# Performance work log

Measured on AMD Instinct MI355X. Metric: run time of the kernel, lower is better.

## Reference

```python
import jax, jax.numpy as jnp
import numpy as np

N_ITEMS = 50000
N_USERS = 20000
N_NODES = N_ITEMS + N_USERS
D = 128
N_REL = 3
NNZ = 800000
K_LAYERS = 2
B, S, L = 256, 4, 50


def setup_inputs() -> dict:
    key = jax.random.key(0)
    ks = iter(jax.random.split(key, 40))
    stdv = float(1.0 / np.sqrt(D))

    def uni(shape):
        return jax.random.uniform(next(ks), shape, jnp.float32, -stdv, stdv)

    id_emb = (jax.random.normal(next(ks), (N_ITEMS, D), jnp.float32) * 0.1).at[0].set(0.0)  # padding_idx=0
    user_emb = jax.random.normal(next(ks), (N_USERS, D), jnp.float32) * 0.1
    inp = dict(
        id_emb=id_emb, user_emb=user_emb,
        lin_r_w=uni((K_LAYERS, N_REL, D, D)),
        upi_w=uni((K_LAYERS, D, D)), upi_b=uni((K_LAYERS, D)),
        upu_w=uni((K_LAYERS, D, D)), upu_b=uni((K_LAYERS, D)),
        w_ih=uni((3 * D, 2 * D)), w_hh=uni((3 * D, D)),
        b_ih=uni((3 * D,)), b_hh=uni((3 * D,)),
        b_iah=uni((D,)), b_oah=uni((D,)),
        ei_w=uni((D, D)), ei_b=uni((D,)),
        eo_w=uni((D, D)), eo_b=uni((D,)),
        q1_w=uni((D, D)), q2_w=uni((D, D)), att_w=uni((D,)),
        fuse_w=uni((D, 2 * D)), fuse_b=uni((D,)),
    )
    # global heterogeneous graph: COO per relation over item+user nodes
    inp['rel_rows'] = jax.random.randint(next(ks), (N_REL, NNZ), 0, N_NODES, dtype=jnp.int32)
    inp['rel_cols'] = jax.random.randint(next(ks), (N_REL, NNZ), 0, N_NODES, dtype=jnp.int32)
    inp['rel_vals'] = jax.random.uniform(next(ks), (N_REL, NNZ), jnp.float32) * 0.1
    # session batch: every session has length in [2, L]
    lens = jax.random.randint(next(ks), (B, S), 2, L + 1)
    raw = jax.random.randint(next(ks), (B, S, L), 1, N_ITEMS)
    inp['ids'] = (raw * (jnp.arange(L)[None, None, :] < lens[:, :, None])).astype(jnp.int32)
    inp['uid'] = jax.random.randint(next(ks), (B,), 0, N_USERS, dtype=jnp.int32)
    inp['u_type'] = jax.random.randint(next(ks), (B,), 0, 3).astype(jnp.float32)
    return inp


def _hgnn(h_item, h_user, rel_rows, rel_cols, rel_vals, lin_r_w, upi_w, upi_b, upu_w, upu_b):
    Ni = h_item.shape[0]
    N = Ni + h_user.shape[0]
    for k in range(lin_r_w.shape[0]):
        h_all = jnp.concatenate([h_item, h_user], 0)
        msg = jnp.zeros_like(h_all)
        for r in range(rel_rows.shape[0]):
            Wh = h_all @ lin_r_w[k, r].T  # per-relation linear
            msg = msg + jax.ops.segment_sum(Wh[rel_cols[r]] * rel_vals[r][:, None],
                                            rel_rows[r], num_segments=N)  # sparse.mm
        h_item = jax.nn.relu((msg[:Ni] + h_item) @ upi_w[k].T + upi_b[k])
        h_user = jax.nn.relu((msg[Ni:] + h_user) @ upu_w[k].T + upu_b[k])
    return h_item, h_user


def reference(id_emb, user_emb, lin_r_w, upi_w, upi_b, upu_w, upu_b,
              w_ih, w_hh, b_ih, b_hh, b_iah, b_oah,
              ei_w, ei_b, eo_w, eo_b, q1_w, q2_w, att_w, fuse_w, fuse_b,
              rel_rows, rel_cols, rel_vals, ids, uid, u_type):
    Bb, Ss, Ll = ids.shape
    N = Ss * Bb
    ids_sb = jnp.transpose(ids, (1, 0, 2)).reshape(N, Ll)  # session-major, matches torch concat order
    lens = (ids_sb != 0).sum(-1)  # >= 2 by construction -> all sessions valid
    rows = jnp.arange(N)
    target = ids_sb[rows, lens - 1]
    Lp = Ll - 1
    m_in = jnp.arange(Lp)[None, :] < (lens - 1)[:, None]
    seq_in = ids_sb[:, :Lp] * m_in
    # session graph: consecutive-item edges; in-half sub-diagonal, out-half super-diagonal
    valid = (m_in[:, 1:] & m_in[:, :-1]).astype(jnp.float32)  # [N, Lp-1]
    i1 = jnp.arange(1, Lp)
    i0 = jnp.arange(Lp - 1)
    a_in = jnp.zeros((N, Lp, Lp), jnp.float32).at[:, i1, i0].set(valid)
    a_out = jnp.zeros((N, Lp, Lp), jnp.float32).at[:, i0, i1].set(valid)
    deg = jnp.clip(a_in.sum(-1), 1.0, None)[..., None]
    a_in = a_in / deg
    a_out = a_out / deg
    h = id_emb[seq_in]  # [N, Lp, D]
    # SessionGNN GRU-style cell (step=1)
    m_i = jnp.matmul(a_in, h @ ei_w.T + ei_b) + b_iah
    m_o = jnp.matmul(a_out, h @ eo_w.T + eo_b) + b_oah
    gi = jnp.concatenate([m_i, m_o], -1) @ w_ih.T + b_ih
    gh = h @ w_hh.T + b_hh
    i_r, i_i, i_n = jnp.split(gi, 3, -1)
    h_r, h_i, h_n = jnp.split(gh, 3, -1)
    rg = jax.nn.sigmoid(i_r + h_r)
    zg = jax.nn.sigmoid(i_i + h_i)
    ng = jnp.tanh(i_n + rg * h_n)
    h = ng + zg * (h - ng)
    # attention readout
    ht = h[rows, jnp.clip(lens - 2, 0, None)]
    alpha = jax.nn.sigmoid((ht @ q1_w.T)[:, None, :] + h @ q2_w.T) @ att_w  # [N, Lp]
    alpha = alpha * m_in.astype(jnp.float32)
    alpha = alpha / (alpha.sum(1, keepdims=True) + 1e-8)
    c_cur = jnp.einsum('nl,nld->nd', alpha, h)
    # global HGNN user context
    g_item, g_user = _hgnn(id_emb[:N_ITEMS], user_emb[:N_USERS], rel_rows, rel_cols,
                           rel_vals, lin_r_w, upi_w, upi_b, upu_w, upu_b)
    c_hist = g_user[jnp.tile(uid, Ss)]
    reps = jnp.concatenate([c_cur, c_hist], -1) @ fuse_w.T + fuse_b
    return reps, target, jnp.tile(u_type, Ss)
```

## Files before the change

kernel.cpp:

```cpp
#include <hip/hip_runtime.h>
#include <hip/hip_bf16.h>

typedef __hip_bfloat16 bf16;
typedef unsigned int uint32;
typedef __attribute__((ext_vector_type(8))) short short8;
typedef __attribute__((ext_vector_type(4))) float f32x4;
typedef __attribute__((ext_vector_type(2))) float f32x2;
typedef __attribute__((ext_vector_type(4))) uint32 u32x4;

#define N_ITEMS_C 50000
#define N_USERS_C 20000
#define N_NODES_C 70000
#define NNZ_C 800000
#define NSESS 1024
#define LP 49
#define NTOK (NSESS * LP)
#define NBK 137

__device__ __forceinline__ float bflo(uint32 u) { return __uint_as_float(u << 16); }
__device__ __forceinline__ float bfhi(uint32 u) { return __uint_as_float(u & 0xffff0000u); }
__device__ __forceinline__ float bfhi_fast(uint32 u) { return __uint_as_float(u); }
__device__ __forceinline__ uint32 packbf(float a, float b) {
    return (uint32)__bfloat16_as_ushort(__float2bfloat16(a)) |
           ((uint32)__bfloat16_as_ushort(__float2bfloat16(b)) << 16);
}

__global__ void init_hab_kernel(const float4* __restrict__ idp, const float4* __restrict__ usp,
                                uint32* __restrict__ hab) {
    int i = blockIdx.x * 256 + threadIdx.x;
    float4 w = (i < 1600000) ? idp[i] : usp[i - 1600000];
    uint2 o = make_uint2(packbf(w.x, w.y), packbf(w.z, w.w));
    *(uint2*)&hab[(size_t)i * 2] = o;
}

__global__ __launch_bounds__(256) void bucket_hist_kernel(
    const int* __restrict__ rel_rows, int* __restrict__ bhist)
{
    __shared__ int hist[NBK];
    const int r = blockIdx.y, tid = threadIdx.x;
    if (tid < NBK) hist[tid] = 0;
    __syncthreads();
    const int* rr = rel_rows + (size_t)r * NNZ_C;
#pragma unroll
    for (int i = 0; i < 16; ++i) {
        int e = blockIdx.x * 4096 + i * 256 + tid;
        if (e < NNZ_C) atomicAdd(&hist[rr[e] >> 9], 1);
    }
    __syncthreads();
    if (tid < NBK && hist[tid]) atomicAdd(&bhist[r * NBK + tid], hist[tid]);
}

__global__ __launch_bounds__(256) void bucket_scan_kernel(
    const int* __restrict__ bhist, int* __restrict__ bbase)
{
    __shared__ int s[256];
    const int tid = threadIdx.x;
    for (int r = 0; r < 3; ++r) {
        s[tid] = (tid < NBK) ? bhist[r * NBK + tid] : 0;
        __syncthreads();
        for (int d = 1; d < 256; d <<= 1) {
            int t = (tid >= d) ? s[tid - d] : 0;
            __syncthreads();
            s[tid] += t;
            __syncthreads();
        }
        if (tid < NBK) bbase[r * (NBK + 1) + tid + 1] = s[tid];
        if (tid == 0) bbase[r * (NBK + 1)] = 0;
        __syncthreads();
    }
}

__global__ __launch_bounds__(256) void bucket_scatter_kernel(
    const int* __restrict__ rel_rows, const int* __restrict__ rel_cols,
    const float* __restrict__ rel_vals, const int* __restrict__ bbase,
    int* __restrict__ cursor, int2* __restrict__ tmp)
{
    __shared__ int hist[NBK], gbase[NBK], cur2[NBK];
    const int r = blockIdx.y, tid = threadIdx.x;
    if (tid < NBK) { hist[tid] = 0; cur2[tid] = 0; }
    __syncthreads();
    const int* rr = rel_rows + (size_t)r * NNZ_C;
    const int* rc = rel_cols + (size_t)r * NNZ_C;
    const float* rv = rel_vals + (size_t)r * NNZ_C;
    int rows[16];
#pragma unroll
    for (int i = 0; i < 16; ++i) {
        int e = blockIdx.x * 4096 + i * 256 + tid;
        rows[i] = (e < NNZ_C) ? rr[e] : -1;
        if (rows[i] >= 0) atomicAdd(&hist[rows[i] >> 9], 1);
    }
    __syncthreads();
    if (tid < NBK)
        gbase[tid] = bbase[r * (NBK + 1) + tid] +
                     (hist[tid] ? atomicAdd(&cursor[r * NBK + tid], hist[tid]) : 0);
    __syncthreads();
    int2* tp = tmp + (size_t)r * NNZ_C;
#pragma unroll
    for (int i = 0; i < 16; ++i) {
        int e = blockIdx.x * 4096 + i * 256 + tid;
        if (rows[i] >= 0) {
            int bk = rows[i] >> 9;
            int rank = atomicAdd(&cur2[bk], 1);
            uint32 fb = __float_as_uint(rv[e]);
            uint32 pk = (uint32)rc[e] | (((fb >> 16) & 0x7FFFu) << 17);
            tp[gbase[bk] + rank] = make_int2((int)pk, rows[i]);
        }
    }
}

__global__ __launch_bounds__(256) void bucket_refine_kernel(
    const int2* __restrict__ tmp, const int* __restrict__ bbase,
    int* __restrict__ offs, uint32* __restrict__ edges)
{
    __shared__ int cnt[512], offsL[512], cur[512];
    __shared__ uint32 outb[6656];
    const int b = blockIdx.x, r = blockIdx.y, tid = threadIdx.x;
    const int lane = tid & 63, wid = tid >> 6;
    const int row0 = b << 9;
    const int e0 = bbase[r * (NBK + 1) + b];
    const int e1 = bbase[r * (NBK + 1) + b + 1];
    cnt[tid] = 0; cnt[256 + tid] = 0; cur[tid] = 0; cur[256 + tid] = 0;
    __syncthreads();
    const int2* tp = tmp + (size_t)r * NNZ_C;
    for (int e = e0 + tid; e < e1; e += 256)
        atomicAdd(&cnt[tp[e].y - row0], 1);
    __syncthreads();
    if (wid == 0) {
        int carry = 0;
        for (int c = 0; c < 8; ++c) {
            int x = cnt[c * 64 + lane];
            int inc = x;
#pragma unroll
            for (int d = 1; d < 64; d <<= 1) {
                int y = __shfl_up(inc, d, 64);
                if (lane >= d) inc += y;
            }
            offsL[c * 64 + lane] = inc - x + carry;
            carry += __shfl(inc, 63, 64);
        }
    }
    __syncthreads();
    for (int i = tid; i < 512; i += 256) {
        int row = row0 + i;
        if (row < 70001) offs[(size_t)r * 70001 + row] = e0 + offsL[i];
    }
    for (int e = e0 + tid; e < e1; e += 256) {
        int2 E = tp[e];
        int lr_ = E.y - row0;
        int slot = offsL[lr_] + atomicAdd(&cur[lr_], 1);
        if (slot < 6656) outb[slot] = (uint32)E.x;
    }
    __syncthreads();
    uint32* eo = edges + (size_t)r * NNZ_C + e0;
    for (int i = tid; i < e1 - e0; i += 256) eo[i] = outb[i];
}

__global__ __launch_bounds__(256) void gather_kernel(
    const uint32* __restrict__ hab, const uint32* __restrict__ edges,
    const int* __restrict__ offs, uint32* __restrict__ T)
{
    const int row = blockIdx.x * 4 + (threadIdx.x >> 6);
    const int lane = threadIdx.x & 63;
    const int grp = lane >> 4;
    const int ql  = lane & 15;
    const char* __restrict__ habB = (const char*)hab + ql * 16;
    f32x2 acc[3][4];
#pragma unroll
    for (int r = 0; r < 3; ++r)
#pragma unroll
        for (int j = 0; j < 4; ++j) acc[r][j] = (f32x2){0.f, 0.f};
#pragma unroll
    for (int r = 0; r < 3; ++r) {
        const uint32* __restrict__ ed = edges + (size_t)r * NNZ_C;
        const int* __restrict__ of = offs + (size_t)r * 70001;
        const int e0 = of[row], e1 = of[row + 1];
        if (e0 >= e1) continue;
        const uint32 span = (uint32)(e1 - e0);
        const int s0 = e0 & ~3;
        for (int eb = s0; eb < e1; eb += 16) {
            const int base = eb + grp * 4;
            uint4 E4 = *(const uint4*)&ed[base];
            uint32 Ej0 = ((uint32)(base + 0 - e0) < span) ? E4.x : 0u;
            uint32 Ej1 = ((uint32)(base + 1 - e0) < span) ? E4.y : 0u;
            uint32 Ej2 = ((uint32)(base + 2 - e0) < span) ? E4.z : 0u;
            uint32 Ej3 = ((uint32)(base + 3 - e0) < span) ? E4.w : 0u;
            uint4 u0 = *(const uint4*)(habB + ((Ej0 & 0x1FFFFu) << 8));
            uint4 u1 = *(const uint4*)(habB + ((Ej1 & 0x1FFFFu) << 8));
            uint4 u2 = *(const uint4*)(habB + ((Ej2 & 0x1FFFFu) << 8));
            uint4 u3 = *(const uint4*)(habB + ((Ej3 & 0x1FFFFu) << 8));
            float v0 = __uint_as_float((Ej0 >> 1) & 0x7FFF0000u);
            float v1 = __uint_as_float((Ej1 >> 1) & 0x7FFF0000u);
            float v2 = __uint_as_float((Ej2 >> 1) & 0x7FFF0000u);
            float v3 = __uint_as_float((Ej3 >> 1) & 0x7FFF0000u);
            f32x2 vv;
            vv = (f32x2){v0, v0};
            acc[r][0] += vv * (f32x2){bflo(u0.x), bfhi_fast(u0.x)};
            acc[r][1] += vv * (f32x2){bflo(u0.y), bfhi_fast(u0.y)};
            acc[r][2] += vv * (f32x2){bflo(u0.z), bfhi_fast(u0.z)};
            acc[r][3] += vv * (f32x2){bflo(u0.w), bfhi_fast(u0.w)};
            vv = (f32x2){v1, v1};
            acc[r][0] += vv * (f32x2){bflo(u1.x), bfhi_fast(u1.x)};
            acc[r][1] += vv * (f32x2){bflo(u1.y), bfhi_fast(u1.y)};
            acc[r][2] += vv * (f32x2){bflo(u1.z), bfhi_fast(u1.z)};
            acc[r][3] += vv * (f32x2){bflo(u1.w), bfhi_fast(u1.w)};
            vv = (f32x2){v2, v2};
            acc[r][0] += vv * (f32x2){bflo(u2.x), bfhi_fast(u2.x)};
            acc[r][1] += vv * (f32x2){bflo(u2.y), bfhi_fast(u2.y)};
            acc[r][2] += vv * (f32x2){bflo(u2.z), bfhi_fast(u2.z)};
            acc[r][3] += vv * (f32x2){bflo(u2.w), bfhi_fast(u2.w)};
            vv = (f32x2){v3, v3};
            acc[r][0] += vv * (f32x2){bflo(u3.x), bfhi_fast(u3.x)};
            acc[r][1] += vv * (f32x2){bflo(u3.y), bfhi_fast(u3.y)};
            acc[r][2] += vv * (f32x2){bflo(u3.z), bfhi_fast(u3.z)};
            acc[r][3] += vv * (f32x2){bflo(u3.w), bfhi_fast(u3.w)};
        }
    }
    float* af = (float*)acc;
#pragma unroll
    for (int off = 16; off < 64; off <<= 1)
#pragma unroll
        for (int j = 0; j < 24; ++j) af[j] += __shfl_xor(af[j], off, 64);
    if (grp == 0) {
#pragma unroll
        for (int r = 0; r < 3; ++r) {
            u32x4 o;
            o.x = packbf(acc[r][0].x, acc[r][0].y);
            o.y = packbf(acc[r][1].x, acc[r][1].y);
            o.z = packbf(acc[r][2].x, acc[r][2].y);
            o.w = packbf(acc[r][3].x, acc[r][3].y);
            __builtin_nontemporal_store(o, (u32x4*)&T[(size_t)row * 192 + r * 64 + ql * 4]);
        }
    }
}

__global__ __launch_bounds__(256, 3) void wprep_kernel(
    const float* __restrict__ upi_w, const float* __restrict__ upu_w,
    const float* __restrict__ lin_r_w, int k, uint32* __restrict__ Wcat)
{
    __shared__ float As[128][65];
    __shared__ __align__(8) bf16 Ws[128][66];
    const int which = blockIdx.y, seg = which / 3, r = which % 3;
    const float* U  = (seg == 0 ? upi_w : upu_w) + (size_t)k * 16384;
    const float* Wr = lin_r_w + (size_t)(k * 3 + r) * 16384;
    uint32* out = Wcat + (size_t)seg * 32768;
    const int tid = threadIdx.x;
    const int row0 = blockIdx.x * 64;
#pragma unroll
    for (int i = 0; i < 8; ++i) {
        int id = i * 256 + tid;
        int rr = id >> 5, c4 = (id & 31) << 2;
        float4 v = *(const float4*)&U[(size_t)(row0 + rr) * 128 + c4];
        As[c4][rr] = v.x; As[c4+1][rr] = v.y; As[c4+2][rr] = v.z; As[c4+3][rr] = v.w;
    }
    const int m0 = (tid & 15) * 4;
    const int n0 = (tid >> 4) * 8;
    float acc[4][8];
#pragma unroll
    for (int i = 0; i < 4; ++i)
#pragma unroll
        for (int j = 0; j < 8; ++j) acc[i][j] = 0.f;
    for (int p = 0; p < 2; ++p) {
        if (p) __syncthreads();
        for (int i = 0; i < 32; ++i) {
            int id = i * 256 + tid;
            int c = id >> 6, kf = id & 63;
            Ws[c][kf] = __float2bfloat16(Wr[(size_t)(p * 64 + kf) * 128 + c]);
        }
        __syncthreads();
        for (int k2 = 0; k2 < 32; ++k2) {
            int kk = p * 64 + 2 * k2;
            float av0[4], av1[4];
#pragma unroll
            for (int i = 0; i < 4; ++i) { av0[i] = As[kk][m0 + i]; av1[i] = As[kk + 1][m0 + i]; }
#pragma unroll
            for (int j = 0; j < 8; ++j) {
                uint32 wp = *(const uint32*)&Ws[n0 + j][2 * k2];
                float w0 = bflo(wp), w1 = bfhi(wp);
#pragma unroll
                for (int i = 0; i < 4; ++i)
                    acc[i][j] = fmaf(av1[i], w1, fmaf(av0[i], w0, acc[i][j]));
            }
        }
    }
#pragma unroll
    for (int i = 0; i < 4; ++i) {
        int n = row0 + m0 + i;
#pragma unroll
        for (int j = 0; j < 8; j += 2)
            out[(size_t)n * 256 + (r * 128 + n0 + j) / 2] = packbf(acc[i][j], acc[i][j + 1]);
    }
}

__global__ __launch_bounds__(256) void upack_kernel(
    const float* __restrict__ upi_w, const float* __restrict__ upu_w,
    int k, uint32* __restrict__ Wcat)
{
    int id = blockIdx.x * 256 + threadIdx.x;
    int seg = id >> 13, p = id & 8191;
    int n = p >> 6, j2 = (p & 63);
    const float* U = (seg ? upu_w : upi_w) + (size_t)k * 16384;
    float2 w = *(const float2*)&U[(size_t)n * 128 + j2 * 2];
    Wcat[(size_t)seg * 32768 + (size_t)n * 256 + 192 + j2] = packbf(w.x, w.y);
}

#define HGNN_ITEM_BLOCKS 391
__global__ __launch_bounds__(256) void hgnn_update_mfma_kernel(
    const bf16* __restrict__ T, uint32* __restrict__ hab,
    const bf16* __restrict__ Wcat, const float* __restrict__ upi_b,
    const float* __restrict__ upu_b, int k)
{
    const int tid = threadIdx.x;
    const int wv = tid >> 6, lane = tid & 63, quad = lane >> 4, lr = lane & 15;
    const int bid = blockIdx.x;
    const int seg = (bid >= HGNN_ITEM_BLOCKS) ? 1 : 0;
    const int row0 = seg ? N_ITEMS_C : 0;
    const int M = seg ? N_USERS_C : N_ITEMS_C;
    const int rbase = (seg ? bid - HGNN_ITEM_BLOCKS : bid) * 128;
    const bf16* __restrict__ Wc = Wcat + (size_t)seg * 65536;
    const float* __restrict__ bias = (seg ? upu_b : upi_b) + k * 128;
    const bf16* hb = (const bf16*)hab;
    f32x4 acc[8][2];
#pragma unroll
    for (int mt = 0; mt < 8; ++mt) { acc[mt][0] = (f32x4){0,0,0,0}; acc[mt][1] = (f32x4){0,0,0,0}; }
    int arow[8];
#pragma unroll
    for (int mt = 0; mt < 8; ++mt) {
        int rr = rbase + mt * 16 + lr;
        arow[mt] = row0 + (rr < M ? rr : M - 1);
    }
#pragma unroll
    for (int ks = 0; ks < 16; ++ks) {
        short8 b0 = *(const short8*)&Wc[(size_t)(wv * 32 + lr) * 512 + ks * 32 + quad * 8];
        short8 b1 = *(const short8*)&Wc[(size_t)(wv * 32 + 16 + lr) * 512 + ks * 32 + quad * 8];
#pragma unroll
        for (int mt = 0; mt < 8; ++mt) {
            short8 a;
            if (ks < 12) a = *(const short8*)&T[(size_t)arow[mt] * 384 + ks * 32 + quad * 8];
            else         a = *(const short8*)&hb[(size_t)arow[mt] * 128 + (ks - 12) * 32 + quad * 8];
            acc[mt][0] = __builtin_amdgcn_mfma_f32_16x16x32_bf16(a, b0, acc[mt][0], 0, 0, 0);
            acc[mt][1] = __builtin_amdgcn_mfma_f32_16x16x32_bf16(a, b1, acc[mt][1], 0, 0, 0);
        }
    }
    __syncthreads();
    unsigned short* hw = (unsigned short*)hab;
#pragma unroll
    for (int s = 0; s < 2; ++s) {
        int col = wv * 32 + s * 16 + lr;
        float bv = bias[col];
#pragma unroll
        for (int mt = 0; mt < 8; ++mt)
#pragma unroll
            for (int reg = 0; reg < 4; ++reg) {
                int rr = rbase + mt * 16 + quad * 4 + reg;
                if (rr < M) {
                    float v = fmaxf(acc[mt][s][reg] + bv, 0.f);
                    hw[(size_t)(row0 + rr) * 128 + col] = __bfloat16_as_ushort(__float2bfloat16(v));
                }
            }
    }
}

__global__ __launch_bounds__(256) void mfma_nt_kernel(
    const bf16* __restrict__ A, const int* __restrict__ rowmap,
    const bf16* __restrict__ W0, const float* __restrict__ b0,
    float* __restrict__ O0, int M)
{
    const int tid = threadIdx.x;
    const int wv = tid >> 6, lane = tid & 63, quad = lane >> 4, lr = lane & 15;
    const int rbase = blockIdx.x * 128;
    int arow[8];
#pragma unroll
    for (int mt = 0; mt < 8; ++mt) {
        int rr = rbase + mt * 16 + lr;
        rr = rr < M ? rr : M - 1;
        arow[mt] = rowmap ? rowmap[rr] : rr;
    }
    f32x4 acc0[8][2];
#pragma unroll
    for (int mt = 0; mt < 8; ++mt) { acc0[mt][0] = (f32x4){0,0,0,0}; acc0[mt][1] = (f32x4){0,0,0,0}; }
#pragma unroll
    for (int ks = 0; ks < 4; ++ks) {
        short8 b00 = *(const short8*)&W0[(size_t)(wv * 32 + lr) * 128 + ks * 32 + quad * 8];
        short8 b01 = *(const short8*)&W0[(size_t)(wv * 32 + 16 + lr) * 128 + ks * 32 + quad * 8];
#pragma unroll
        for (int mt = 0; mt < 8; ++mt) {
            short8 a = *(const short8*)&A[(size_t)arow[mt] * 128 + ks * 32 + quad * 8];
            acc0[mt][0] = __builtin_amdgcn_mfma_f32_16x16x32_bf16(a, b00, acc0[mt][0], 0, 0, 0);
            acc0[mt][1] = __builtin_amdgcn_mfma_f32_16x16x32_bf16(a, b01, acc0[mt][1], 0, 0, 0);
        }
    }
#pragma unroll
    for (int s = 0; s < 2; ++s) {
        int col = wv * 32 + s * 16 + lr;
        float bv0 = b0 ? b0[col] : 0.f;
#pragma unroll
        for (int mt = 0; mt < 8; ++mt)
#pragma unroll
            for (int reg = 0; reg < 4; ++reg) {
                int rr = rbase + mt * 16 + quad * 4 + reg;
                if (rr < M) O0[(size_t)rr * 128 + col] = acc0[mt][s][reg] + bv0;
            }
    }
}

__global__ __launch_bounds__(256) void mfma_agi_kernel(
    const bf16* __restrict__ A,
    const bf16* __restrict__ Wi, const bf16* __restrict__ Wo,
    const float* __restrict__ ei_b, const float* __restrict__ eo_b,
    const float* __restrict__ b_iah, const float* __restrict__ b_oah,
    const int* __restrict__ lens, unsigned short* __restrict__ AgiG)
{
    const int tid = threadIdx.x;
    const int wv = tid >> 6, lane = tid & 63, quad = lane >> 4, lr = lane & 15;
    const int rbase = blockIdx.x * 32;
    int arow[2];
#pragma unroll
    for (int mt = 0; mt < 2; ++mt) arow[mt] = rbase + mt * 16 + lr;
    f32x4 acc0[2][2], acc1[2][2];
#pragma unroll
    for (int mt = 0; mt < 2; ++mt) {
        acc0[mt][0] = (f32x4){0,0,0,0}; acc0[mt][1] = (f32x4){0,0,0,0};
        acc1[mt][0] = (f32x4){0,0,0,0}; acc1[mt][1] = (f32x4){0,0,0,0};
    }
#pragma unroll
    for (int ks = 0; ks < 4; ++ks) {
        short8 b00 = *(const short8*)&Wi[(size_t)(wv * 32 + lr) * 128 + ks * 32 + quad * 8];
        short8 b01 = *(const short8*)&Wi[(size_t)(wv * 32 + 16 + lr) * 128 + ks * 32 + quad * 8];
        short8 b10 = *(const short8*)&Wo[(size_t)(wv * 32 + lr) * 128 + ks * 32 + quad * 8];
        short8 b11 = *(const short8*)&Wo[(size_t)(wv * 32 + 16 + lr) * 128 + ks * 32 + quad * 8];
#pragma unroll
        for (int mt = 0; mt < 2; ++mt) {
            short8 a = *(const short8*)&A[(size_t)arow[mt] * 128 + ks * 32 + quad * 8];
            acc0[mt][0] = __builtin_amdgcn_mfma_f32_16x16x32_bf16(a, b00, acc0[mt][0], 0, 0, 0);
            acc0[mt][1] = __builtin_amdgcn_mfma_f32_16x16x32_bf16(a, b01, acc0[mt][1], 0, 0, 0);
            acc1[mt][0] = __builtin_amdgcn_mfma_f32_16x16x32_bf16(a, b10, acc1[mt][0], 0, 0, 0);
            acc1[mt][1] = __builtin_amdgcn_mfma_f32_16x16x32_bf16(a, b11, acc1[mt][1], 0, 0, 0);
        }
    }
#pragma unroll
    for (int s = 0; s < 2; ++s) {
        int col = wv * 32 + s * 16 + lr;
        float bei = ei_b[col], beo = eo_b[col];
        float bia = b_iah[col], boa = b_oah[col];
#pragma unroll
        for (int mt = 0; mt < 2; ++mt)
#pragma unroll
            for (int reg = 0; reg < 4; ++reg) {
                int rr = rbase + mt * 16 + quad * 4 + reg;
                int d1 = rr + 1; if (d1 == NTOK) d1 = 0;
                int n1 = d1 / LP, t1 = d1 - n1 * LP, l1 = lens[n1];
                float v1 = bia + ((t1 >= 1 && t1 < l1 - 1) ? acc0[mt][s][reg] + bei : 0.f);
                AgiG[(size_t)d1 * 256 + col] = __bfloat16_as_ushort(__float2bfloat16(v1));
                int d2 = rr - 1; if (d2 < 0) d2 = NTOK - 1;
                int n2 = d2 / LP, t2 = d2 - n2 * LP, l2 = lens[n2];
                float v2 = boa + ((t2 < l2 - 2) ? acc1[mt][s][reg] + beo : 0.f);
                AgiG[(size_t)d2 * 256 + 128 + col] = __bfloat16_as_ushort(__float2bfloat16(v2));
            }
    }
}

__global__ void session_prep_kernel(const int* __restrict__ ids, const int* __restrict__ uid,
                                    const float* __restrict__ u_type,
                                    int* __restrict__ lens, int* __restrict__ rowmap,
                                    float* __restrict__ out_target, float* __restrict__ out_utype)
{
    int n = blockIdx.x * 256 + threadIdx.x;
    if (n >= NSESS) return;
    int b = n & 255, s = n >> 8;
    const int* row = ids + (size_t)(b * 4 + s) * 50;
    int len = 0;
#pragma unroll
    for (int l = 0; l < 50; ++l) len += (row[l] != 0) ? 1 : 0;
    lens[n] = len;
    rowmap[n] = n * LP + (len - 2);
    out_target[n] = (float)row[len - 1];
    out_utype[n] = u_type[b];
}

__global__ void chist_kernel(const uint32* __restrict__ hab, const int* __restrict__ uid,
                             float* __restrict__ chist) {
    int n = blockIdx.x, d = threadIdx.x;
    uint32 u = hab[(size_t)(N_ITEMS_C + uid[n & 255]) * 64 + (d >> 1)];
    chist[(size_t)n * 128 + d] = (d & 1) ? bfhi(u) : bflo(u);
}

__global__ __launch_bounds__(256) void h0_gather_kernel(
    const float* __restrict__ id_emb, const int* __restrict__ ids,
    const int* __restrict__ lens, uint32* __restrict__ hb) {
    int g = blockIdx.x * 4 + (threadIdx.x >> 6);
    int d = threadIdx.x & 63;
    int n = g / LP;
    int tt = g - n * LP;
    int len = lens[n];
    int b = n & 255, s = n >> 8;
    int id = (tt < len - 1) ? ids[(size_t)(b * 4 + s) * 50 + tt] : 0;
    float2 e = *(const float2*)&id_emb[(size_t)id * 128 + d * 2];
    hb[(size_t)g * 64 + d] = packbf(e.x, e.y);
}

__global__ __launch_bounds__(256) void epack_kernel(
    const float* __restrict__ w_ih, const float* __restrict__ w_hh,
    const float* __restrict__ ei_w, const float* __restrict__ eo_w,
    const float* __restrict__ q2_w, const float* __restrict__ q1_w,
    const float* __restrict__ fuse_w, uint32* __restrict__ dst)
{
    int id = blockIdx.x * 256 + threadIdx.x;
    if (id >= 106496) {
        if (id >= 139264) return;
        int f = id - 106496;
        int kk = f >> 7, n = f & 127;
        ((float*)dst)[id] = fuse_w[(size_t)n * 256 + kk];
        return;
    }
    const float* src; int off;
    if      (id <  49152) { src = w_ih; off = id; }
    else if (id <  73728) { src = w_hh; off = id - 49152; }
    else if (id <  81920) { src = ei_w; off = id - 73728; }
    else if (id <  90112) { src = eo_w; off = id - 81920; }
    else if (id <  98304) { src = q2_w; off = id - 90112; }
    else                  { src = q1_w; off = id - 98304; }
    float2 w = *(const float2*)&src[(size_t)off * 2];
    dst[id] = packbf(w.x, w.y);
}

__global__ __launch_bounds__(256, 2) void gru_mfma_kernel(
    const bf16* __restrict__ Agi,
    uint32* __restrict__ hb,
    const bf16* __restrict__ wihb,
    const bf16* __restrict__ whhb,
    const float* __restrict__ b_ih, const float* __restrict__ b_hh)
{
    const int tid = threadIdx.x;
    const int wv = tid >> 6;
    const int lane = tid & 63;
    const int quad = lane >> 4;
    const int lr = lane & 15;
    const int c0 = wv * 32;
    const int g0 = blockIdx.x * 32;
    int arow[2];
#pragma unroll
    for (int mt = 0; mt < 2; ++mt) arow[mt] = g0 + mt * 16 + lr;

    f32x4 acc[2][2][4];
#pragma unroll
    for (int mt = 0; mt < 2; ++mt)
#pragma unroll
        for (int s = 0; s < 2; ++s)
#pragma unroll
            for (int j = 0; j < 4; ++j) acc[mt][s][j] = (f32x4){0.f, 0.f, 0.f, 0.f};

#pragma unroll 2
    for (int ks = 0; ks < 8; ++ks) {
        short8 bfr[2][3];
#pragma unroll
        for (int s = 0; s < 2; ++s)
#pragma unroll
            for (int gte = 0; gte < 3; ++gte) {
                int n0 = gte * 128 + c0 + s * 16 + lr;
                bfr[s][gte] = *(const short8*)&wihb[(size_t)n0 * 256 + ks * 32 + quad * 8];
            }
#pragma unroll
        for (int mt = 0; mt < 2; ++mt) {
            short8 a = *(const short8*)&Agi[(size_t)arow[mt] * 256 + ks * 32 + quad * 8];
#pragma unroll
            for (int s = 0; s < 2; ++s) {
                acc[mt][s][0] = __builtin_amdgcn_mfma_f32_16x16x32_bf16(a, bfr[s][0], acc[mt][s][0], 0, 0, 0);
                acc[mt][s][1] = __builtin_amdgcn_mfma_f32_16x16x32_bf16(a, bfr[s][1], acc[mt][s][1], 0, 0, 0);
                acc[mt][s][2] = __builtin_amdgcn_mfma_f32_16x16x32_bf16(a, bfr[s][2], acc[mt][s][2], 0, 0, 0);
            }
        }
    }
    const bf16* hbb = (const bf16*)hb;
#pragma unroll 2
    for (int ks = 0; ks < 4; ++ks) {
        short8 bfr[2][3];
#pragma unroll
        for (int s = 0; s < 2; ++s)
#pragma unroll
            for (int gte = 0; gte < 3; ++gte) {
                int n0 = gte * 128 + c0 + s * 16 + lr;
                bfr[s][gte] = *(const short8*)&whhb[(size_t)n0 * 128 + ks * 32 + quad * 8];
            }
#pragma unroll
        for (int mt = 0; mt < 2; ++mt) {
            short8 a = *(const short8*)&hbb[(size_t)arow[mt] * 128 + ks * 32 + quad * 8];
#pragma unroll
            for (int s = 0; s < 2; ++s) {
                acc[mt][s][0] = __builtin_amdgcn_mfma_f32_16x16x32_bf16(a, bfr[s][0], acc[mt][s][0], 0, 0, 0);
                acc[mt][s][1] = __builtin_amdgcn_mfma_f32_16x16x32_bf16(a, bfr[s][1], acc[mt][s][1], 0, 0, 0);
                acc[mt][s][3] = __builtin_amdgcn_mfma_f32_16x16x32_bf16(a, bfr[s][2], acc[mt][s][3], 0, 0, 0);
            }
        }
    }

    __syncthreads();
    unsigned short* hu = (unsigned short*)hb;
#pragma unroll
    for (int s = 0; s < 2; ++s) {
        int col = c0 + s * 16 + lr;
        float brz = b_ih[col] + b_hh[col];
        float bzz = b_ih[col + 128] + b_hh[col + 128];
        float bin = b_ih[col + 256];
        float bhn = b_hh[col + 256];
#pragma unroll
        for (int mt = 0; mt < 2; ++mt)
#pragma unroll
            for (int reg = 0; reg < 4; ++reg) {
                int row = g0 + mt * 16 + quad * 4 + reg;
                float rg = 1.f / (1.f + expf(-(acc[mt][s][0][reg] + brz)));
                float zg = 1.f / (1.f + expf(-(acc[mt][s][1][reg] + bzz)));
                float ng = tanhf(acc[mt][s][2][reg] + bin + rg * (acc[mt][s][3][reg] + bhn));
                size_t idx = (size_t)row * 128 + col;
                float ho = __uint_as_float((uint32)hu[idx] << 16);
                hu[idx] = __bfloat16_as_ushort(__float2bfloat16(ng + zg * (ho - ng)));
            }
    }
}

__global__ __launch_bounds__(256) void alpha_kernel(
    const float* __restrict__ q1h, const float* __restrict__ q2h,
    const float* __restrict__ att_w, const int* __restrict__ lens,
    float* __restrict__ al)
{
    int tok = blockIdx.x * 4 + (threadIdx.x >> 6);
    int lane = threadIdx.x & 63;
    int n = tok / LP, t = tok - n * LP;
    int len = lens[n];
    float2 q2 = *(const float2*)&q2h[(size_t)tok * 128 + lane * 2];
    float2 q1 = *(const float2*)&q1h[(size_t)n * 128 + lane * 2];
    float2 aw = *(const float2*)&att_w[lane * 2];
    float s = aw.x / (1.f + expf(-(q1.x + q2.x))) + aw.y / (1.f + expf(-(q1.y + q2.y)));
#pragma unroll
    for (int off = 1; off < 64; off <<= 1) s += __shfl_xor(s, off, 64);
    if (lane == 0) al[tok] = (t < len - 1) ? s : 0.f;
}

__global__ __launch_bounds__(128) void attn_fuse_kernel(
    const float* __restrict__ alG, const unsigned short* __restrict__ hu,
    const float* __restrict__ chist, const int* __restrict__ lens,
    const float* __restrict__ ftwf, const float* __restrict__ fuse_b,
    float* __restrict__ out)
{
    __shared__ float al[64], cv[256];
    const int n = blockIdx.x, tid = threadIdx.x;
    if (tid < 64) al[tid] = (tid < LP) ? alG[(size_t)n * LP + tid] : 0.f;
    __syncthreads();
    const int len = lens[n];
    float ssum = 0.f;
    for (int t = 0; t < len - 1; ++t) ssum += al[t];
    float inv = 1.f / (ssum + 1e-8f);
    float c = 0.f;
    for (int t = 0; t < len - 1; ++t) {
        float hv = __uint_as_float((uint32)hu[(size_t)(n * LP + t) * 128 + tid] << 16);
        c += al[t] * inv * hv;
    }
    cv[tid] = c;
    cv[128 + tid] = chist[(size_t)n * 128 + tid];
    __syncthreads();
    float s = fuse_b[tid];
    for (int kk = 0; kk < 256; ++kk)
        s += cv[kk] * ftwf[(size_t)kk * 128 + tid];
    out[(size_t)n * 128 + tid] = s;
}

extern "C" void kernel_launch(void* const* d_in, const int* in_sizes, int n_in,
                              void* d_out, int out_size, void* d_ws, size_t ws_size,
                              hipStream_t stream)
{
    const float* id_emb   = (const float*)d_in[0];
    const float* user_emb = (const float*)d_in[1];
    const float* lin_r_w  = (const float*)d_in[2];
    const float* upi_w    = (const float*)d_in[3];
    const float* upi_b    = (const float*)d_in[4];
    const float* upu_w    = (const float*)d_in[5];
    const float* upu_b    = (const float*)d_in[6];
    const float* w_ih     = (const float*)d_in[7];
    const float* w_hh     = (const float*)d_in[8];
    const float* b_ih     = (const float*)d_in[9];
    const float* b_hh     = (const float*)d_in[10];
    const float* b_iah    = (const float*)d_in[11];
    const float* b_oah    = (const float*)d_in[12];
    const float* ei_w     = (const float*)d_in[13];
    const float* ei_b     = (const float*)d_in[14];
    const float* eo_w     = (const float*)d_in[15];
    const float* eo_b     = (const float*)d_in[16];
    const float* q1_w     = (const float*)d_in[17];
    const float* q2_w     = (const float*)d_in[18];
    const float* att_w    = (const float*)d_in[19];
    const float* fuse_w   = (const float*)d_in[20];
    const float* fuse_b   = (const float*)d_in[21];
    const int*  rel_rows  = (const int*)d_in[22];
    const int*  rel_cols  = (const int*)d_in[23];
    const float* rel_vals = (const float*)d_in[24];
    const int*  ids       = (const int*)d_in[25];
    const int*  uid       = (const int*)d_in[26];
    const float* u_type   = (const float*)d_in[27];
    float* out = (float*)d_out;

    uint32* W32    = (uint32*)d_ws;
    uint32* hab    = W32;
    uint32* T      = W32 + 4480000;
    uint32* edges  = W32 + 17920000;
    int2*   tmp    = (int2*)(W32 + 20320000);
    int*    offs   = (int*)(W32 + 25120000);
    int*    bhist  = (int*)(W32 + 25330004);
    int*    cursor = (int*)(W32 + 25330415);
    int*    bbase  = (int*)(W32 + 25330826);
    uint32* Wcat   = W32 + 25331240;
    float*  q1h    = (float*)(W32 + 25396776);
    float*  chist  = (float*)(W32 + 25527848);
    int*    lens   = (int*)(W32 + 25658920);
    int*    rowmap = (int*)(W32 + 25659944);
    float*  alG    = (float*)(W32 + 25660968);
    uint32* sess_hb = W32;
    float* q2h      = (float*)(W32 + 4480000);
    unsigned short* AgiG = (unsigned short*)(W32 + 10902528);
    uint32* wpk     = W32 + 17920000;
    uint32* wihb = wpk;
    uint32* whhb = wpk + 49152;
    uint32* eiwb = wpk + 73728;
    uint32* eowb = wpk + 81920;
    uint32* q2wb = wpk + 90112;
    uint32* q1wb = wpk + 98304;
    float*  ftwf = (float*)(wpk + 106496);
    if (ws_size < (size_t)27144192 * 4 + 4096) return;

    init_hab_kernel<<<8750, 256, 0, stream>>>((const float4*)id_emb, (const float4*)user_emb, hab);
    hipMemsetAsync(bhist, 0, (size_t)822 * 4, stream);
    bucket_hist_kernel<<<dim3(196, 3), 256, 0, stream>>>(rel_rows, bhist);
    bucket_scan_kernel<<<1, 256, 0, stream>>>(bhist, bbase);
    bucket_scatter_kernel<<<dim3(196, 3), 256, 0, stream>>>(rel_rows, rel_cols, rel_vals,
                                                            bbase, cursor, tmp);
    bucket_refine_kernel<<<dim3(NBK, 3), 256, 0, stream>>>(tmp, bbase, offs, edges);

    for (int k = 0; k < 2; ++k) {
        wprep_kernel<<<dim3(2, 6), 256, 0, stream>>>(upi_w, upu_w, lin_r_w, k, Wcat);
        upack_kernel<<<64, 256, 0, stream>>>(upi_w, upu_w, k, Wcat);
        gather_kernel<<<17500, 256, 0, stream>>>(hab, edges, offs, T);
        hgnn_update_mfma_kernel<<<548, 256, 0, stream>>>((const bf16*)T, hab,
            (const bf16*)Wcat, upi_b, upu_b, k);
    }

    session_prep_kernel<<<4, 256, 0, stream>>>(ids, uid, u_type, lens, rowmap,
        out + 131072, out + 132096);
    chist_kernel<<<NSESS, 128, 0, stream>>>(hab, uid, chist);
    epack_kernel<<<544, 256, 0, stream>>>(w_ih, w_hh, ei_w, eo_w, q2_w, q1_w, fuse_w, wpk);
    h0_gather_kernel<<<NTOK / 4, 256, 0, stream>>>(id_emb, ids, lens, sess_hb);
    mfma_agi_kernel<<<1568, 256, 0, stream>>>((const bf16*)sess_hb,
        (const bf16*)eiwb, (const bf16*)eowb, ei_b, eo_b, b_iah, b_oah, lens, AgiG);
    gru_mfma_kernel<<<1568, 256, 0, stream>>>((const bf16*)AgiG, sess_hb,
        (const bf16*)wihb, (const bf16*)whhb, b_ih, b_hh);
    mfma_nt_kernel<<<392, 256, 0, stream>>>((const bf16*)sess_hb, nullptr,
        (const bf16*)q2wb, nullptr, q2h, NTOK);
    mfma_nt_kernel<<<8, 256, 0, stream>>>((const bf16*)sess_hb, rowmap,
        (const bf16*)q1wb, nullptr, q1h, NSESS);
    alpha_kernel<<<NTOK / 4, 256, 0, stream>>>(q1h, q2h, att_w, lens, alG);
    attn_fuse_kernel<<<NSESS, 128, 0, stream>>>(alG, (const unsigned short*)sess_hb,
        chist, lens, ftwf, fuse_b, out);
}
```

Baseline: 755.1 us.

## Fuse shifted edge-linear Agi computation into GRU kernel via shared memory

Merges the separate mfma_agi kernel into the GRU kernel. Each block recomputes the ei/eo projections for its 32 rows plus halo tiles and writes the shifted, masked Agi rows into LDS instead of a global bf16 buffer. The GRU output now goes to a separate hb2 buffer to avoid read/write races across blocks, and downstream kernels read hb2. This removes a kernel launch and a global round trip of the Agi intermediate. In exchange it does redundant halo MFMA work (3 tiles instead of 2) and drops the 2-blocks-per-CU launch bound hint.

```diff
diff --git a/kernel.cpp b/kernel.cpp
--- a/kernel.cpp
+++ b/kernel.cpp
@@ -403,62 +403,6 @@
     }
 }
 
-__global__ __launch_bounds__(256) void mfma_agi_kernel(
-    const bf16* __restrict__ A,
-    const bf16* __restrict__ Wi, const bf16* __restrict__ Wo,
-    const float* __restrict__ ei_b, const float* __restrict__ eo_b,
-    const float* __restrict__ b_iah, const float* __restrict__ b_oah,
-    const int* __restrict__ lens, unsigned short* __restrict__ AgiG)
-{
-    const int tid = threadIdx.x;
-    const int wv = tid >> 6, lane = tid & 63, quad = lane >> 4, lr = lane & 15;
-    const int rbase = blockIdx.x * 32;
-    int arow[2];
-#pragma unroll
-    for (int mt = 0; mt < 2; ++mt) arow[mt] = rbase + mt * 16 + lr;
-    f32x4 acc0[2][2], acc1[2][2];
-#pragma unroll
-    for (int mt = 0; mt < 2; ++mt) {
-        acc0[mt][0] = (f32x4){0,0,0,0}; acc0[mt][1] = (f32x4){0,0,0,0};
-        acc1[mt][0] = (f32x4){0,0,0,0}; acc1[mt][1] = (f32x4){0,0,0,0};
-    }
-#pragma unroll
-    for (int ks = 0; ks < 4; ++ks) {
-        short8 b00 = *(const short8*)&Wi[(size_t)(wv * 32 + lr) * 128 + ks * 32 + quad * 8];
-        short8 b01 = *(const short8*)&Wi[(size_t)(wv * 32 + 16 + lr) * 128 + ks * 32 + quad * 8];
-        short8 b10 = *(const short8*)&Wo[(size_t)(wv * 32 + lr) * 128 + ks * 32 + quad * 8];
-        short8 b11 = *(const short8*)&Wo[(size_t)(wv * 32 + 16 + lr) * 128 + ks * 32 + quad * 8];
-#pragma unroll
-        for (int mt = 0; mt < 2; ++mt) {
-            short8 a = *(const short8*)&A[(size_t)arow[mt] * 128 + ks * 32 + quad * 8];
-            acc0[mt][0] = __builtin_amdgcn_mfma_f32_16x16x32_bf16(a, b00, acc0[mt][0], 0, 0, 0);
-            acc0[mt][1] = __builtin_amdgcn_mfma_f32_16x16x32_bf16(a, b01, acc0[mt][1], 0, 0, 0);
-            acc1[mt][0] = __builtin_amdgcn_mfma_f32_16x16x32_bf16(a, b10, acc1[mt][0], 0, 0, 0);
-            acc1[mt][1] = __builtin_amdgcn_mfma_f32_16x16x32_bf16(a, b11, acc1[mt][1], 0, 0, 0);
-        }
-    }
-#pragma unroll
-    for (int s = 0; s < 2; ++s) {
-        int col = wv * 32 + s * 16 + lr;
-        float bei = ei_b[col], beo = eo_b[col];
-        float bia = b_iah[col], boa = b_oah[col];
-#pragma unroll
-        for (int mt = 0; mt < 2; ++mt)
-#pragma unroll
-            for (int reg = 0; reg < 4; ++reg) {
-                int rr = rbase + mt * 16 + quad * 4 + reg;
-                int d1 = rr + 1; if (d1 == NTOK) d1 = 0;
-                int n1 = d1 / LP, t1 = d1 - n1 * LP, l1 = lens[n1];
-                float v1 = bia + ((t1 >= 1 && t1 < l1 - 1) ? acc0[mt][s][reg] + bei : 0.f);
-                AgiG[(size_t)d1 * 256 + col] = __bfloat16_as_ushort(__float2bfloat16(v1));
-                int d2 = rr - 1; if (d2 < 0) d2 = NTOK - 1;
-                int n2 = d2 / LP, t2 = d2 - n2 * LP, l2 = lens[n2];
-                float v2 = boa + ((t2 < l2 - 2) ? acc1[mt][s][reg] + beo : 0.f);
-                AgiG[(size_t)d2 * 256 + 128 + col] = __bfloat16_as_ushort(__float2bfloat16(v2));
-            }
-    }
-}
-
 __global__ void session_prep_kernel(const int* __restrict__ ids, const int* __restrict__ uid,
                                     const float* __restrict__ u_type,
                                     int* __restrict__ lens, int* __restrict__ rowmap,
@@ -523,13 +467,18 @@
     dst[id] = packbf(w.x, w.y);
 }
 
-__global__ __launch_bounds__(256, 2) void gru_mfma_kernel(
-    const bf16* __restrict__ Agi,
-    uint32* __restrict__ hb,
+__global__ __launch_bounds__(256) void gru_fused_kernel(
+    const uint32* __restrict__ hb,
+    unsigned short* __restrict__ hb2,
+    const bf16* __restrict__ Wi, const bf16* __restrict__ Wo,
     const bf16* __restrict__ wihb,
     const bf16* __restrict__ whhb,
-    const float* __restrict__ b_ih, const float* __restrict__ b_hh)
-{
+    const float* __restrict__ ei_b, const float* __restrict__ eo_b,
+    const float* __restrict__ b_iah, const float* __restrict__ b_oah,
+    const float* __restrict__ b_ih, const float* __restrict__ b_hh,
+    const int* __restrict__ lens)
+{
+    __shared__ __align__(16) bf16 Agi[32][264];
     const int tid = threadIdx.x;
     const int wv = tid >> 6;
     const int lane = tid & 63;
@@ -537,10 +486,72 @@
     const int lr = lane & 15;
     const int c0 = wv * 32;
     const int g0 = blockIdx.x * 32;
+    const bf16* hbb = (const bf16*)hb;
+
+    int arows[4];
+#pragma unroll
+    for (int t = 0; t < 4; ++t) {
+        int r = g0 + (t - 1) * 16 + lr;
+        arows[t] = (r < 0) ? r + NTOK : (r >= NTOK ? r - NTOK : r);
+    }
+    f32x4 aEi[3][2], aEo[3][2];
+#pragma unroll
+    for (int t = 0; t < 3; ++t) {
+        aEi[t][0] = (f32x4){0,0,0,0}; aEi[t][1] = (f32x4){0,0,0,0};
+        aEo[t][0] = (f32x4){0,0,0,0}; aEo[t][1] = (f32x4){0,0,0,0};
+    }
+#pragma unroll
+    for (int ks = 0; ks < 4; ++ks) {
+        short8 bi0 = *(const short8*)&Wi[(size_t)(wv * 32 + lr) * 128 + ks * 32 + quad * 8];
+        short8 bi1 = *(const short8*)&Wi[(size_t)(wv * 32 + 16 + lr) * 128 + ks * 32 + quad * 8];
+        short8 bo0 = *(const short8*)&Wo[(size_t)(wv * 32 + lr) * 128 + ks * 32 + quad * 8];
+        short8 bo1 = *(const short8*)&Wo[(size_t)(wv * 32 + 16 + lr) * 128 + ks * 32 + quad * 8];
+        short8 a[4];
+#pragma unroll
+        for (int t = 0; t < 4; ++t)
+            a[t] = *(const short8*)&hbb[(size_t)arows[t] * 128 + ks * 32 + quad * 8];
+#pragma unroll
+        for (int t = 0; t < 3; ++t) {
+            aEi[t][0] = __builtin_amdgcn_mfma_f32_16x16x32_bf16(a[t], bi0, aEi[t][0], 0, 0, 0);
+            aEi[t][1] = __builtin_amdgcn_mfma_f32_16x16x32_bf16(a[t], bi1, aEi[t][1], 0, 0, 0);
+            aEo[t][0] = __builtin_amdgcn_mfma_f32_16x16x32_bf16(a[t + 1], bo0, aEo[t][0], 0, 0, 0);
+            aEo[t][1] = __builtin_amdgcn_mfma_f32_16x16x32_bf16(a[t + 1], bo1, aEo[t][1], 0, 0, 0);
+        }
+    }
+#pragma unroll
+    for (int s = 0; s < 2; ++s) {
+        int col = c0 + s * 16 + lr;
+        float bei = ei_b[col], beo = eo_b[col];
+        float bia = b_iah[col], boa = b_oah[col];
+#pragma unroll
+        for (int t = 0; t < 3; ++t)
+#pragma unroll
+            for (int reg = 0; reg < 4; ++reg) {
+                int src = g0 + (t - 1) * 16 + quad * 4 + reg;
+                int ssrc = (src < 0) ? src + NTOK : (src >= NTOK ? src - NTOK : src);
+                int d1 = ssrc + 1; if (d1 == NTOK) d1 = 0;
+                int ld = d1 - g0;
+                if ((unsigned)ld < 32u) {
+                    int n1 = d1 / LP, t1 = d1 - n1 * LP, l1 = lens[n1];
+                    float v = bia + ((t1 >= 1 && t1 < l1 - 1) ? aEi[t][s][reg] + bei : 0.f);
+                    Agi[ld][col] = __float2bfloat16(v);
+                }
+                int src2 = g0 + t * 16 + quad * 4 + reg;
+                int ssrc2 = (src2 >= NTOK) ? src2 - NTOK : src2;
+                int d2 = (ssrc2 == 0) ? NTOK - 1 : ssrc2 - 1;
+                int ld2 = d2 - g0;
+                if ((unsigned)ld2 < 32u) {
+                    int n2 = d2 / LP, t2 = d2 - n2 * LP, l2 = lens[n2];
+                    float v = boa + ((t2 < l2 - 2) ? aEo[t][s][reg] + beo : 0.f);
+                    Agi[ld2][128 + col] = __float2bfloat16(v);
+                }
+            }
+    }
+    __syncthreads();
+
     int arow[2];
 #pragma unroll
     for (int mt = 0; mt < 2; ++mt) arow[mt] = g0 + mt * 16 + lr;
-
     f32x4 acc[2][2][4];
 #pragma unroll
     for (int mt = 0; mt < 2; ++mt)
@@ -561,7 +572,7 @@
             }
 #pragma unroll
         for (int mt = 0; mt < 2; ++mt) {
-            short8 a = *(const short8*)&Agi[(size_t)arow[mt] * 256 + ks * 32 + quad * 8];
+            short8 a = *(const short8*)&Agi[mt * 16 + lr][ks * 32 + quad * 8];
 #pragma unroll
             for (int s = 0; s < 2; ++s) {
                 acc[mt][s][0] = __builtin_amdgcn_mfma_f32_16x16x32_bf16(a, bfr[s][0], acc[mt][s][0], 0, 0, 0);
@@ -570,7 +581,6 @@
             }
         }
     }
-    const bf16* hbb = (const bf16*)hb;
 #pragma unroll 2
     for (int ks = 0; ks < 4; ++ks) {
         short8 bfr[2][3];
@@ -593,8 +603,7 @@
         }
     }
 
-    __syncthreads();
-    unsigned short* hu = (unsigned short*)hb;
+    const unsigned short* hold = (const unsigned short*)hb;
 #pragma unroll
     for (int s = 0; s < 2; ++s) {
         int col = c0 + s * 16 + lr;
@@ -611,8 +620,8 @@
                 float zg = 1.f / (1.f + expf(-(acc[mt][s][1][reg] + bzz)));
                 float ng = tanhf(acc[mt][s][2][reg] + bin + rg * (acc[mt][s][3][reg] + bhn));
                 size_t idx = (size_t)row * 128 + col;
-                float ho = __uint_as_float((uint32)hu[idx] << 16);
-                hu[idx] = __bfloat16_as_ushort(__float2bfloat16(ng + zg * (ho - ng)));
+                float ho = __uint_as_float((uint32)hold[idx] << 16);
+                hb2[idx] = __bfloat16_as_ushort(__float2bfloat16(ng + zg * (ho - ng)));
             }
     }
 }
@@ -714,7 +723,7 @@
     float*  alG    = (float*)(W32 + 25660968);
     uint32* sess_hb = W32;
     float* q2h      = (float*)(W32 + 4480000);
-    unsigned short* AgiG = (unsigned short*)(W32 + 10902528);
+    unsigned short* hb2 = (unsigned short*)(W32 + 10902528);
     uint32* wpk     = W32 + 17920000;
     uint32* wihb = wpk;
     uint32* whhb = wpk + 49152;
@@ -746,15 +755,15 @@
     chist_kernel<<<NSESS, 128, 0, stream>>>(hab, uid, chist);
     epack_kernel<<<544, 256, 0, stream>>>(w_ih, w_hh, ei_w, eo_w, q2_w, q1_w, fuse_w, wpk);
     h0_gather_kernel<<<NTOK / 4, 256, 0, stream>>>(id_emb, ids, lens, sess_hb);
-    mfma_agi_kernel<<<1568, 256, 0, stream>>>((const bf16*)sess_hb,
-        (const bf16*)eiwb, (const bf16*)eowb, ei_b, eo_b, b_iah, b_oah, lens, AgiG);
-    gru_mfma_kernel<<<1568, 256, 0, stream>>>((const bf16*)AgiG, sess_hb,
-        (const bf16*)wihb, (const bf16*)whhb, b_ih, b_hh);
-    mfma_nt_kernel<<<392, 256, 0, stream>>>((const bf16*)sess_hb, nullptr,
+    gru_fused_kernel<<<1568, 256, 0, stream>>>(sess_hb, hb2,
+        (const bf16*)eiwb, (const bf16*)eowb,
+        (const bf16*)wihb, (const bf16*)whhb,
+        ei_b, eo_b, b_iah, b_oah, b_ih, b_hh, lens);
+    mfma_nt_kernel<<<392, 256, 0, stream>>>((const bf16*)hb2, nullptr,
         (const bf16*)q2wb, nullptr, q2h, NTOK);
-    mfma_nt_kernel<<<8, 256, 0, stream>>>((const bf16*)sess_hb, rowmap,
+    mfma_nt_kernel<<<8, 256, 0, stream>>>((const bf16*)hb2, rowmap,
         (const bf16*)q1wb, nullptr, q1h, NSESS);
     alpha_kernel<<<NTOK / 4, 256, 0, stream>>>(q1h, q2h, att_w, lens, alG);
-    attn_fuse_kernel<<<NSESS, 128, 0, stream>>>(alG, (const unsigned short*)sess_hb,
+    attn_fuse_kernel<<<NSESS, 128, 0, stream>>>(alG, (const unsigned short*)hb2,
         chist, lens, ftwf, fuse_b, out);
 }
```

Measured after the change: 748.2 us. About the same (-0.9%).
